# Optimization experiments

Hardware: AMD Instinct MI355X
Metric: run time of the kernel (lower is better)

The kernel has to match this reference:

```python
import jax, jax.numpy as jnp
import numpy as np

# Sizes (see shape_source)
N_P, N_C, E = 65536, 8192, 131072
D_P, D_C, D_ADD, D_EDGE, D_HID = 80, 48, 16, 8, 64
F_IN = D_P + D_C + D_ADD  # 144, message_input_irreps dim


def setup_inputs() -> dict:
    key = jax.random.key(0)
    ks = jax.random.split(key, 8)
    x_p = jax.random.normal(ks[0], (N_P, D_P), jnp.float32)
    x_c = jax.random.normal(ks[1], (N_C, D_C), jnp.float32)
    src = jax.random.randint(ks[2], (E,), 0, N_C)  # indexes x_c (edge_index[0])
    dst = jax.random.randint(ks[3], (E,), 0, N_P)  # indexes x_p (edge_index[1])
    edge_index = jnp.stack([src, dst], axis=0)
    edge_attr = jax.random.normal(ks[4], (E, D_EDGE), jnp.float32)
    additional_message_features = jax.random.normal(ks[5], (E, D_ADD), jnp.float32)
    batch = jnp.zeros((N_P,), jnp.int32)  # single graph; unused when norm=None
    # Fully-connected tensor-product weights (scalar irreps -> bilinear map) + scalar bias
    W1 = jax.random.normal(ks[6], (F_IN, D_EDGE, D_HID), jnp.float32) / np.float32(np.sqrt(F_IN * D_EDGE))
    b1 = jnp.zeros((D_HID,), jnp.float32)
    W2 = jax.random.normal(ks[7], (D_HID, D_EDGE, D_HID), jnp.float32) / np.float32(np.sqrt(D_HID * D_EDGE))
    b2 = jnp.zeros((D_HID,), jnp.float32)
    return {"x_p": x_p, "x_c": x_c, "edge_index": edge_index, "edge_attr": edge_attr,
            "batch": batch, "additional_message_features": additional_message_features,
            "W1": W1, "b1": b1, "W2": W2, "b2": b2}


def _tp(x, a, W, b):
    """Fully-connected O3 tensor product on scalar irreps: out[e,h] = sum_{f,g} x[e,f] a[e,g] W[f,g,h] + b[h]."""
    # contract feature axis first to avoid the [E, F, G] outer product
    y = (x @ W.reshape(W.shape[0], -1)).reshape(x.shape[0], a.shape[1], -1)  # [E, G, H]
    return jnp.einsum('eg,egh->eh', a, y) + b


def reference(x_p, x_c, edge_index, edge_attr, batch, additional_message_features, W1, b1, W2, b2):
    src, dst = edge_index[0], edge_index[1]
    # gather: [E, D_P + D_C + D_ADD]
    inp = jnp.concatenate([x_p[dst], x_c[src], additional_message_features], axis=-1)
    # two O3TensorProductSwishGate message layers (scalar irreps -> bilinear + swish)
    m = jax.nn.silu(_tp(inp, edge_attr, W1, b1))
    m = jax.nn.silu(_tp(m, edge_attr, W2, b2))
    # scatter-sum over destination (particle) nodes, then concat with residual features
    agg = jax.ops.segment_sum(m, dst, num_segments=x_p.shape[0])
    return jnp.concatenate([x_p, agg], axis=-1)  # [N_P, D_P + D_HID]
```

## Files before the change

kernel.cpp:

```cpp
#include <hip/hip_runtime.h>
#include <hip/hip_bf16.h>

#define E_CNT 131072
#define NP_CNT 65536
#define D_P 80
#define D_C 48
#define D_ADD 16
#define K1 1152
#define K2 512

typedef _Float16 f16x8 __attribute__((ext_vector_type(8)));
typedef _Float16 f16x4 __attribute__((ext_vector_type(4)));
typedef _Float16 f16x2 __attribute__((ext_vector_type(2)));
typedef float f32x4 __attribute__((ext_vector_type(4)));

__device__ __forceinline__ float silu_f(float x){
  return x / (1.0f + __expf(-x));
}
__device__ __forceinline__ f16x2 pkrtz(float a, float b){
  return __builtin_bit_cast(f16x2, __builtin_amdgcn_cvt_pkrtz(a, b));
}

__global__ void prep_w_kernel(const float* __restrict__ W1, const float* __restrict__ W2,
                              _Float16* __restrict__ wt1, _Float16* __restrict__ wt2){
  int id = blockIdx.x * 256 + threadIdx.x;
  if (id < 64 * K1){
    int h = id / K1;
    int k = id - h * K1;
    wt1[id] = (_Float16)W1[k * 64 + h];
  } else {
    int id2 = id - 64 * K1;
    int h = id2 / K2;
    int k = id2 - h * K2;
    wt2[id2] = (_Float16)W2[k * 64 + h];
  }
}

__global__ void init_out_kernel(const float4* __restrict__ xp4, float4* __restrict__ out4){
  int i4 = blockIdx.x * 256 + threadIdx.x;
  int row = i4 / 36;
  int jq = i4 - row * 36;
  float4 z = make_float4(0.f, 0.f, 0.f, 0.f);
  out4[i4] = (jq < 20) ? xp4[row * 20 + jq] : z;
}

template<int KTOT, bool SECOND>
__global__ __launch_bounds__(256, 4) void msg_gemm_kernel(
    const float* __restrict__ x_p, const float* __restrict__ x_c,
    const int* __restrict__ eidx, const float* __restrict__ ea,
    const float* __restrict__ addf,
    const _Float16* __restrict__ wt, const float* __restrict__ bias,
    const _Float16* __restrict__ m1in,
    _Float16* __restrict__ m1out,
    float* __restrict__ out)
{
  __shared__ unsigned int s_xa[128 * 32];
  __shared__ unsigned int s_w [64 * 32];
  __shared__ int s_dst[128];

  const int t    = threadIdx.x;
  const int er   = t >> 1;
  const int hh   = t & 1;
  const int e    = blockIdx.x * 128 + er;
  const int lane = t & 63;
  const int wv   = t >> 6;
  const int l15  = lane & 15;
  const int q    = lane >> 4;

  f16x2 apk[4];
  {
    const float4* ap = reinterpret_cast<const float4*>(ea + (size_t)e * 8);
    float4 a0 = ap[0], a1 = ap[1];
    apk[0] = pkrtz(a0.x, a0.y);
    apk[1] = pkrtz(a0.z, a0.w);
    apk[2] = pkrtz(a1.x, a1.y);
    apk[3] = pkrtz(a1.z, a1.w);
  }
  const int dstI = eidx[E_CNT + e];
  int srcI = 0;
  if constexpr (!SECOND) srcI = eidx[e];
  if constexpr (SECOND)  s_dst[er] = dstI;

  f32x4 acc[2][4];
  #pragma unroll
  for (int i = 0; i < 2; ++i)
    #pragma unroll
    for (int j = 0; j < 4; ++j)
      acc[i][j] = f32x4{0.f, 0.f, 0.f, 0.f};

  constexpr int NCH = KTOT / 64;
  for (int c = 0; c < NCH; ++c){
    uint4 wreg[2];
    const int wh = t >> 2, wpart = t & 3;
    {
      const _Float16* gw = wt + (size_t)wh * KTOT + c * 64;
      #pragma unroll
      for (int qq = 0; qq < 2; ++qq)
        wreg[qq] = *reinterpret_cast<const uint4*>(gw + (wpart * 2 + qq) * 8);
    }
    f16x2 xbc[4];
    if constexpr (!SECOND){
      const int fb = c * 8 + hh * 4;
      const float* src;
      if (fb < D_P)            src = x_p  + (size_t)dstI * D_P   + fb;
      else if (fb < D_P + D_C) src = x_c  + (size_t)srcI * D_C   + (fb - D_P);
      else                     src = addf + (size_t)e    * D_ADD + (fb - D_P - D_C);
      float4 v = *reinterpret_cast<const float4*>(src);
      xbc[0] = pkrtz(v.x, v.x);
      xbc[1] = pkrtz(v.y, v.y);
      xbc[2] = pkrtz(v.z, v.z);
      xbc[3] = pkrtz(v.w, v.w);
    } else {
      const _Float16* mp = m1in + (size_t)e * 64 + c * 8 + hh * 4;
      f16x4 mh = __builtin_bit_cast(f16x4, *reinterpret_cast<const uint2*>(mp));
      #pragma unroll
      for (int j = 0; j < 4; ++j){ xbc[j] = f16x2{mh[j], mh[j]}; }
    }
    #pragma unroll
    for (int fl = 0; fl < 4; ++fl){
      f16x2 p0 = xbc[fl] * apk[0];
      f16x2 p1 = xbc[fl] * apk[1];
      f16x2 p2 = xbc[fl] * apk[2];
      f16x2 p3 = xbc[fl] * apk[3];
      uint4 w4;
      w4.x = __builtin_bit_cast(unsigned, p0);
      w4.y = __builtin_bit_cast(unsigned, p1);
      w4.z = __builtin_bit_cast(unsigned, p2);
      w4.w = __builtin_bit_cast(unsigned, p3);
      const int slot = (hh * 4 + fl) ^ (er & 7);
      *reinterpret_cast<uint4*>(&s_xa[er * 32 + slot * 4]) = w4;
    }
    #pragma unroll
    for (int qq = 0; qq < 2; ++qq){
      const int sl = wpart * 2 + qq;
      const int phys = sl ^ (wh & 7);
      *reinterpret_cast<uint4*>(&s_w[wh * 32 + phys * 4]) = wreg[qq];
    }
    __syncthreads();
    #pragma unroll
    for (int ks = 0; ks < 2; ++ks){
      f16x8 Af[2], Bf[4];
      #pragma unroll
      for (int mt = 0; mt < 2; ++mt){
        const int erow = wv * 32 + mt * 16 + l15;
        const int slot = (ks * 4 + q) ^ (erow & 7);
        Af[mt] = __builtin_bit_cast(f16x8, *reinterpret_cast<const uint4*>(&s_xa[erow * 32 + slot * 4]));
      }
      #pragma unroll
      for (int nt = 0; nt < 4; ++nt){
        const int hr = nt * 16 + l15;
        const int slot = (ks * 4 + q) ^ (hr & 7);
        Bf[nt] = __builtin_bit_cast(f16x8, *reinterpret_cast<const uint4*>(&s_w[hr * 32 + slot * 4]));
      }
      #pragma unroll
      for (int mt = 0; mt < 2; ++mt)
        #pragma unroll
        for (int nt = 0; nt < 4; ++nt)
          acc[mt][nt] = __builtin_amdgcn_mfma_f32_16x16x32_f16(Af[mt], Bf[nt], acc[mt][nt], 0, 0, 0);
    }
    __syncthreads();
  }

  float bv[4];
  #pragma unroll
  for (int nt = 0; nt < 4; ++nt) bv[nt] = bias[nt * 16 + l15];

  #pragma unroll
  for (int mt = 0; mt < 2; ++mt){
    #pragma unroll
    for (int nt = 0; nt < 4; ++nt){
      #pragma unroll
      for (int r = 0; r < 4; ++r){
        float x = acc[mt][nt][r] + bv[nt];
        float s = silu_f(x);
        const int erow = wv * 32 + mt * 16 + q * 4 + r;
        if constexpr (!SECOND){
          m1out[(size_t)(blockIdx.x * 128 + erow) * 64 + nt * 16 + l15] = (_Float16)s;
        } else {
          unsafeAtomicAdd(out + (size_t)s_dst[erow] * 144 + 80 + nt * 16 + l15, s);
        }
      }
    }
  }
}

extern "C" void kernel_launch(void* const* d_in, const int* in_sizes, int n_in,
                              void* d_out, int out_size, void* d_ws, size_t ws_size,
                              hipStream_t stream){
  const float* x_p  = (const float*)d_in[0];
  const float* x_c  = (const float*)d_in[1];
  const int*   eidx = (const int*)d_in[2];
  const float* ea   = (const float*)d_in[3];
  const float* addf = (const float*)d_in[5];
  const float* W1   = (const float*)d_in[6];
  const float* b1   = (const float*)d_in[7];
  const float* W2   = (const float*)d_in[8];
  const float* b2   = (const float*)d_in[9];
  float* out = (float*)d_out;

  char* ws = (char*)d_ws;
  _Float16* wt1 = (_Float16*)(ws);
  _Float16* wt2 = (_Float16*)(ws + 163840);
  _Float16* m1  = (_Float16*)(ws + 262144);

  prep_w_kernel<<<(64 * K1 + 64 * K2) / 256, 256, 0, stream>>>(W1, W2, wt1, wt2);
  init_out_kernel<<<(NP_CNT * 36) / 256, 256, 0, stream>>>((const float4*)x_p, (float4*)out);
  msg_gemm_kernel<K1, false><<<E_CNT / 128, 256, 0, stream>>>(
      x_p, x_c, eidx, ea, addf, wt1, b1, nullptr, m1, nullptr);
  msg_gemm_kernel<K2, true><<<E_CNT / 128, 256, 0, stream>>>(
      x_p, x_c, eidx, ea, addf, wt2, b2, m1, nullptr, out);
}
```

Before: 91.84 us.

## Keep whole weight matrix in LDS and build A fragments in registers

Each block now handles 512 edges with 512 threads and loads the full transposed fp16 weight matrix into padded dynamic shared memory once. The A operand (x outer edge_attr) is formed directly in registers per MFMA, so the per-chunk LDS staging of A and the two barriers per chunk are gone. Feature gathers are scalar loads prefetched four k-steps ahead through a register ring. This removes LDS round-trips and synchronisation, at the cost of a large LDS footprint (about 148 KB for layer 1), which limits occupancy, plus many more scalar uncoalesced gather loads and high register pressure from 8x2 accumulators and prefetch buffers.

```diff
diff --git a/kernel.cpp b/kernel.cpp
--- a/kernel.cpp
+++ b/kernel.cpp
@@ -10,9 +10,10 @@
 #define K2 512
 
 typedef _Float16 f16x8 __attribute__((ext_vector_type(8)));
-typedef _Float16 f16x4 __attribute__((ext_vector_type(4)));
 typedef _Float16 f16x2 __attribute__((ext_vector_type(2)));
 typedef float f32x4 __attribute__((ext_vector_type(4)));
+
+union F16x8U { f16x2 h2[4]; f16x8 v8; };
 
 __device__ __forceinline__ float silu_f(float x){
   return x / (1.0f + __expf(-x));
@@ -45,139 +46,134 @@
 }
 
 template<int KTOT, bool SECOND>
-__global__ __launch_bounds__(256, 4) void msg_gemm_kernel(
+__global__ __launch_bounds__(512, 2) void msg_gemm_kernel(
     const float* __restrict__ x_p, const float* __restrict__ x_c,
     const int* __restrict__ eidx, const float* __restrict__ ea,
     const float* __restrict__ addf,
     const _Float16* __restrict__ wt, const float* __restrict__ bias,
-    const _Float16* __restrict__ m1in,
+    const unsigned short* __restrict__ m1in,
     _Float16* __restrict__ m1out,
     float* __restrict__ out)
 {
-  __shared__ unsigned int s_xa[128 * 32];
-  __shared__ unsigned int s_w [64 * 32];
-  __shared__ int s_dst[128];
+  extern __shared__ _Float16 s_w[];
+  __shared__ int s_dst[512];
+  constexpr int ROW = KTOT + 8;
+  constexpr int NKS = KTOT / 32;
+  constexpr int KCH = KTOT / 8;
 
   const int t    = threadIdx.x;
-  const int er   = t >> 1;
-  const int hh   = t & 1;
-  const int e    = blockIdx.x * 128 + er;
   const int lane = t & 63;
   const int wv   = t >> 6;
+  const int wm   = wv >> 1;
+  const int wn   = wv & 1;
   const int l15  = lane & 15;
   const int q    = lane >> 4;
 
-  f16x2 apk[4];
-  {
+  for (int i = t; i < 64 * KCH; i += 512){
+    int h = i / KCH, p = i - h * KCH;
+    *reinterpret_cast<uint4*>(&s_w[h * ROW + p * 8]) =
+        *reinterpret_cast<const uint4*>(wt + h * KTOT + p * 8);
+  }
+  if constexpr (SECOND) s_dst[t] = eidx[E_CNT + blockIdx.x * 512 + t];
+
+  const int ebase = blockIdx.x * 512 + wm * 128;
+
+  int iP[8], iC[8], iA[8], iM[8];
+  f16x2 apk[8][4];
+  #pragma unroll
+  for (int mt = 0; mt < 8; ++mt){
+    const int e = ebase + mt * 16 + l15;
+    if constexpr (!SECOND){
+      const int d = eidx[E_CNT + e];
+      const int s = eidx[e];
+      iP[mt] = d * D_P + q;
+      iC[mt] = s * D_C + q;
+      iA[mt] = e * D_ADD + q;
+      iM[mt] = 0;
+    } else {
+      iM[mt] = e * 64 + q;
+      iP[mt] = iC[mt] = iA[mt] = 0;
+    }
     const float4* ap = reinterpret_cast<const float4*>(ea + (size_t)e * 8);
     float4 a0 = ap[0], a1 = ap[1];
-    apk[0] = pkrtz(a0.x, a0.y);
-    apk[1] = pkrtz(a0.z, a0.w);
-    apk[2] = pkrtz(a1.x, a1.y);
-    apk[3] = pkrtz(a1.z, a1.w);
-  }
-  const int dstI = eidx[E_CNT + e];
-  int srcI = 0;
-  if constexpr (!SECOND) srcI = eidx[e];
-  if constexpr (SECOND)  s_dst[er] = dstI;
-
-  f32x4 acc[2][4];
-  #pragma unroll
-  for (int i = 0; i < 2; ++i)
-    #pragma unroll
-    for (int j = 0; j < 4; ++j)
-      acc[i][j] = f32x4{0.f, 0.f, 0.f, 0.f};
-
-  constexpr int NCH = KTOT / 64;
-  for (int c = 0; c < NCH; ++c){
-    uint4 wreg[2];
-    const int wh = t >> 2, wpart = t & 3;
-    {
-      const _Float16* gw = wt + (size_t)wh * KTOT + c * 64;
+    apk[mt][0] = pkrtz(a0.x, a0.y);
+    apk[mt][1] = pkrtz(a0.z, a0.w);
+    apk[mt][2] = pkrtz(a1.x, a1.y);
+    apk[mt][3] = pkrtz(a1.z, a1.w);
+  }
+
+  f32x4 acc[8][2];
+  #pragma unroll
+  for (int mt = 0; mt < 8; ++mt){
+    acc[mt][0] = f32x4{0.f,0.f,0.f,0.f};
+    acc[mt][1] = f32x4{0.f,0.f,0.f,0.f};
+  }
+
+  float    xf[4][8];
+  unsigned xu[4][8];
+
+  const int wb = (wn * 32 + l15) * ROW + q * 8;
+
+  auto FETCH = [&](int ks, int sl){
+    #pragma unroll
+    for (int mt = 0; mt < 8; ++mt){
+      if constexpr (!SECOND){
+        if (ks < 20)      xf[sl][mt] = x_p [iP[mt] + ks * 4];
+        else if (ks < 32) xf[sl][mt] = x_c [iC[mt] + (ks - 20) * 4];
+        else              xf[sl][mt] = addf[iA[mt] + (ks - 32) * 4];
+      } else {
+        xu[sl][mt] = m1in[iM[mt] + ks * 4];
+      }
+    }
+  };
+
+  FETCH(0, 0); FETCH(1, 1); FETCH(2, 2); FETCH(3, 3);
+  __syncthreads();
+
+  #pragma unroll
+  for (int ks = 0; ks < NKS; ++ks){
+    const int sl = ks & 3;
+    f16x8 Bf[2];
+    #pragma unroll
+    for (int nt = 0; nt < 2; ++nt)
+      Bf[nt] = __builtin_bit_cast(f16x8,
+          *reinterpret_cast<const uint4*>(&s_w[wb + nt * 16 * ROW + ks * 32]));
+    #pragma unroll
+    for (int mt = 0; mt < 8; ++mt){
+      f16x2 xb;
+      if constexpr (!SECOND){
+        float xvv = xf[sl][mt];
+        xb = pkrtz(xvv, xvv);
+      } else {
+        unsigned uu = xu[sl][mt];
+        xb = __builtin_bit_cast(f16x2, (uu << 16) | uu);
+      }
+      F16x8U A;
       #pragma unroll
-      for (int qq = 0; qq < 2; ++qq)
-        wreg[qq] = *reinterpret_cast<const uint4*>(gw + (wpart * 2 + qq) * 8);
-    }
-    f16x2 xbc[4];
-    if constexpr (!SECOND){
-      const int fb = c * 8 + hh * 4;
-      const float* src;
-      if (fb < D_P)            src = x_p  + (size_t)dstI * D_P   + fb;
-      else if (fb < D_P + D_C) src = x_c  + (size_t)srcI * D_C   + (fb - D_P);
-      else                     src = addf + (size_t)e    * D_ADD + (fb - D_P - D_C);
-      float4 v = *reinterpret_cast<const float4*>(src);
-      xbc[0] = pkrtz(v.x, v.x);
-      xbc[1] = pkrtz(v.y, v.y);
-      xbc[2] = pkrtz(v.z, v.z);
-      xbc[3] = pkrtz(v.w, v.w);
-    } else {
-      const _Float16* mp = m1in + (size_t)e * 64 + c * 8 + hh * 4;
-      f16x4 mh = __builtin_bit_cast(f16x4, *reinterpret_cast<const uint2*>(mp));
-      #pragma unroll
-      for (int j = 0; j < 4; ++j){ xbc[j] = f16x2{mh[j], mh[j]}; }
-    }
-    #pragma unroll
-    for (int fl = 0; fl < 4; ++fl){
-      f16x2 p0 = xbc[fl] * apk[0];
-      f16x2 p1 = xbc[fl] * apk[1];
-      f16x2 p2 = xbc[fl] * apk[2];
-      f16x2 p3 = xbc[fl] * apk[3];
-      uint4 w4;
-      w4.x = __builtin_bit_cast(unsigned, p0);
-      w4.y = __builtin_bit_cast(unsigned, p1);
-      w4.z = __builtin_bit_cast(unsigned, p2);
-      w4.w = __builtin_bit_cast(unsigned, p3);
-      const int slot = (hh * 4 + fl) ^ (er & 7);
-      *reinterpret_cast<uint4*>(&s_xa[er * 32 + slot * 4]) = w4;
-    }
-    #pragma unroll
-    for (int qq = 0; qq < 2; ++qq){
-      const int sl = wpart * 2 + qq;
-      const int phys = sl ^ (wh & 7);
-      *reinterpret_cast<uint4*>(&s_w[wh * 32 + phys * 4]) = wreg[qq];
-    }
-    __syncthreads();
-    #pragma unroll
-    for (int ks = 0; ks < 2; ++ks){
-      f16x8 Af[2], Bf[4];
-      #pragma unroll
-      for (int mt = 0; mt < 2; ++mt){
-        const int erow = wv * 32 + mt * 16 + l15;
-        const int slot = (ks * 4 + q) ^ (erow & 7);
-        Af[mt] = __builtin_bit_cast(f16x8, *reinterpret_cast<const uint4*>(&s_xa[erow * 32 + slot * 4]));
-      }
-      #pragma unroll
-      for (int nt = 0; nt < 4; ++nt){
-        const int hr = nt * 16 + l15;
-        const int slot = (ks * 4 + q) ^ (hr & 7);
-        Bf[nt] = __builtin_bit_cast(f16x8, *reinterpret_cast<const uint4*>(&s_w[hr * 32 + slot * 4]));
-      }
-      #pragma unroll
-      for (int mt = 0; mt < 2; ++mt)
-        #pragma unroll
-        for (int nt = 0; nt < 4; ++nt)
-          acc[mt][nt] = __builtin_amdgcn_mfma_f32_16x16x32_f16(Af[mt], Bf[nt], acc[mt][nt], 0, 0, 0);
-    }
-    __syncthreads();
-  }
-
-  float bv[4];
-  #pragma unroll
-  for (int nt = 0; nt < 4; ++nt) bv[nt] = bias[nt * 16 + l15];
-
-  #pragma unroll
-  for (int mt = 0; mt < 2; ++mt){
-    #pragma unroll
-    for (int nt = 0; nt < 4; ++nt){
+      for (int j = 0; j < 4; ++j) A.h2[j] = xb * apk[mt][j];
+      acc[mt][0] = __builtin_amdgcn_mfma_f32_16x16x32_f16(A.v8, Bf[0], acc[mt][0], 0, 0, 0);
+      acc[mt][1] = __builtin_amdgcn_mfma_f32_16x16x32_f16(A.v8, Bf[1], acc[mt][1], 0, 0, 0);
+    }
+    if (ks + 4 < NKS) FETCH(ks + 4, sl);
+  }
+
+  float bv[2];
+  bv[0] = bias[wn * 32 + l15];
+  bv[1] = bias[wn * 32 + 16 + l15];
+
+  #pragma unroll
+  for (int mt = 0; mt < 8; ++mt){
+    #pragma unroll
+    for (int nt = 0; nt < 2; ++nt){
       #pragma unroll
       for (int r = 0; r < 4; ++r){
-        float x = acc[mt][nt][r] + bv[nt];
-        float s = silu_f(x);
-        const int erow = wv * 32 + mt * 16 + q * 4 + r;
+        float s = silu_f(acc[mt][nt][r] + bv[nt]);
+        const int eo = wm * 128 + mt * 16 + q * 4 + r;
+        const int h  = wn * 32 + nt * 16 + l15;
         if constexpr (!SECOND){
-          m1out[(size_t)(blockIdx.x * 128 + erow) * 64 + nt * 16 + l15] = (_Float16)s;
+          m1out[(size_t)(blockIdx.x * 512 + eo) * 64 + h] = (_Float16)s;
         } else {
-          unsafeAtomicAdd(out + (size_t)s_dst[erow] * 144 + 80 + nt * 16 + l15, s);
+          unsafeAtomicAdd(out + (size_t)s_dst[eo] * 144 + 80 + h, s);
         }
       }
     }
@@ -203,10 +199,17 @@
   _Float16* wt2 = (_Float16*)(ws + 163840);
   _Float16* m1  = (_Float16*)(ws + 262144);
 
+  constexpr int SH1 = 64 * (K1 + 8) * 2;
+  constexpr int SH2 = 64 * (K2 + 8) * 2;
+  hipFuncSetAttribute(reinterpret_cast<const void*>(msg_gemm_kernel<K1, false>),
+                      hipFuncAttributeMaxDynamicSharedMemorySize, SH1);
+  hipFuncSetAttribute(reinterpret_cast<const void*>(msg_gemm_kernel<K2, true>),
+                      hipFuncAttributeMaxDynamicSharedMemorySize, SH2);
+
   prep_w_kernel<<<(64 * K1 + 64 * K2) / 256, 256, 0, stream>>>(W1, W2, wt1, wt2);
   init_out_kernel<<<(NP_CNT * 36) / 256, 256, 0, stream>>>((const float4*)x_p, (float4*)out);
-  msg_gemm_kernel<K1, false><<<E_CNT / 128, 256, 0, stream>>>(
+  msg_gemm_kernel<K1, false><<<E_CNT / 512, 512, SH1, stream>>>(
       x_p, x_c, eidx, ea, addf, wt1, b1, nullptr, m1, nullptr);
-  msg_gemm_kernel<K2, true><<<E_CNT / 128, 256, 0, stream>>>(
-      x_p, x_c, eidx, ea, addf, wt2, b2, m1, nullptr, out);
-}
+  msg_gemm_kernel<K2, true><<<E_CNT / 512, 512, SH2, stream>>>(
+      x_p, x_c, eidx, ea, addf, wt2, b2, (const unsigned short*)m1, nullptr, out);
+}
```

Result: slower. 138.6 us (+50.9%).
